# Kernel optimization log

Measured on AMD Instinct MI355X. Metric: run time of the kernel, lower is better.

## Reference

```python
import jax, jax.numpy as jnp
import numpy as np

B, T, H = 16, 2048, 1024

def setup_inputs() -> dict:
    key = jax.random.key(0)
    k1, k2, k3, k4 = jax.random.split(key, 4)
    stdv = 1.0 / np.sqrt(H)
    return {
        "hidden": jax.random.normal(k1, (B, H), dtype=jnp.float32),
        "encoder_outputs": jax.random.normal(k2, (B, T, 2 * H), dtype=jnp.float32),
        "W": jax.random.normal(k3, (H, 3 * H), dtype=jnp.float32) * stdv,  # nn.Linear(3H, H) weight
        "b": jnp.zeros((H,), dtype=jnp.float32),
        "v": jax.random.normal(k4, (H,), dtype=jnp.float32) * stdv,
    }

def reference(hidden, encoder_outputs, W, b, v):
    # hidden: (B,H); encoder_outputs: (B,T,2H)
    Bsz, Tlen, _ = encoder_outputs.shape
    Hrep = jnp.broadcast_to(hidden[:, None, :], (Bsz, Tlen, hidden.shape[-1]))  # (B,T,H)
    cat = jnp.concatenate([Hrep, encoder_outputs], axis=2)                      # (B,T,3H)
    energy = jnp.tanh(jnp.einsum('btk,hk->bth', cat, W) + b)                    # (B,T,H)
    scores = jnp.einsum('bth,h->bt', energy, v)[:, None, :]                     # (B,1,T), == bmm(v, energy^T)
    return jax.nn.softmax(scores, axis=2)
```

## Files before the change

kernel.cpp:

```cpp
#include <hip/hip_runtime.h>
#include <cstdint>

#define B_SZ 16
#define T_SZ 2048
#define H_SZ 1024
#define K_SZ 2048
#define M_SZ (B_SZ * T_SZ)

#define BM 128
#define BN 128
#define BK 64
#define LDK 72
#define KTILES (K_SZ / BK)

typedef _Float16 half8_t __attribute__((ext_vector_type(8)));
typedef float float4_t __attribute__((ext_vector_type(4)));

__device__ __forceinline__ void glds16(const _Float16* g, _Float16* l) {
    __builtin_amdgcn_global_load_lds(
        (const __attribute__((address_space(1))) void*)g,
        (__attribute__((address_space(3))) void*)l, 16, 0, 0);
}

__global__ __launch_bounds__(256) void cvt_enc_kernel(
    const float* __restrict__ src, _Float16* __restrict__ dst) {
    size_t i = ((size_t)blockIdx.x * 256 + threadIdx.x) * 8;
    float4_t a = *(const float4_t*)(src + i);
    float4_t b = *(const float4_t*)(src + i + 4);
    half8_t h;
    h[0] = (_Float16)a[0]; h[1] = (_Float16)a[1];
    h[2] = (_Float16)a[2]; h[3] = (_Float16)a[3];
    h[4] = (_Float16)b[0]; h[5] = (_Float16)b[1];
    h[6] = (_Float16)b[2]; h[7] = (_Float16)b[3];
    *(half8_t*)(dst + i) = h;
}

__global__ __launch_bounds__(256) void cvt_w2_kernel(
    const float* __restrict__ W, _Float16* __restrict__ dst) {
    int idx8 = blockIdx.x * 256 + threadIdx.x;
    int n = idx8 >> 8, k = (idx8 & 255) * 8;
    const float* src = W + (size_t)n * 3072 + H_SZ + k;
    float4_t a = *(const float4_t*)(src);
    float4_t b = *(const float4_t*)(src + 4);
    half8_t h;
    h[0] = (_Float16)a[0]; h[1] = (_Float16)a[1];
    h[2] = (_Float16)a[2]; h[3] = (_Float16)a[3];
    h[4] = (_Float16)b[0]; h[5] = (_Float16)b[1];
    h[6] = (_Float16)b[2]; h[7] = (_Float16)b[3];
    int nblk = n >> 4, m16 = n & 15;
    int kblk = k >> 5, quad = (k >> 3) & 3;
    size_t di = (((size_t)nblk * 64 + kblk) * 64 + quad * 16 + m16) * 8;
    *(half8_t*)(dst + di) = h;
}

__global__ __launch_bounds__(256) void hpart_kernel(
    const float* __restrict__ hidden, const float* __restrict__ W,
    const float* __restrict__ bias, float* __restrict__ hpart) {
    int wave = (blockIdx.x * 256 + threadIdx.x) >> 6;
    int lane = threadIdx.x & 63;
    int b = wave >> 10;
    int h = wave & 1023;
    const float* wrow = W + (size_t)h * 3072;
    const float* hrow = hidden + b * H_SZ;
    int k0 = lane * 16;
    float acc = 0.f;
#pragma unroll
    for (int j = 0; j < 4; ++j) {
        float4_t wv = *(const float4_t*)(wrow + k0 + j * 4);
        float4_t hv = *(const float4_t*)(hrow + k0 + j * 4);
        acc += wv[0] * hv[0] + wv[1] * hv[1] + wv[2] * hv[2] + wv[3] * hv[3];
    }
#pragma unroll
    for (int off = 32; off >= 1; off >>= 1) acc += __shfl_xor(acc, off, 64);
    if (lane == 0) hpart[b * H_SZ + h] = acc + bias[h];
}

__global__ __launch_bounds__(256, 4) void attn_gemm16_kernel(
    const _Float16* __restrict__ A, const _Float16* __restrict__ Bp,
    const float* __restrict__ hpart, const float* __restrict__ v,
    float* __restrict__ partial) {
    __shared__ _Float16 Af[BM * BK];
    __shared__ float hp_s[BN];
    __shared__ float v_s[BN];

    const int bidx = blockIdx.x;
    const int blockN = bidx & 7;
    const int blockM = bidx >> 3;
    const int tid = threadIdx.x;
    const int lane = tid & 63;
    const int w = tid >> 6;
    const int wm = w & 1, wn = w >> 1;
    const int m16 = lane & 15, quad = lane >> 4;
    const int sw = m16 & 7;

    const int n0 = blockN * BN;
    const int batch = blockM >> 4;

    if (tid < BN) {
        hp_s[tid] = hpart[batch * H_SZ + n0 + tid];
        v_s[tid] = v[n0 + tid];
    }

    float4_t acc[4][4];
#pragma unroll
    for (int i = 0; i < 4; ++i)
#pragma unroll
        for (int j = 0; j < 4; ++j) acc[i][j] = (float4_t){0.f, 0.f, 0.f, 0.f};

    const _Float16* Abase = A + (size_t)(blockM * BM) * K_SZ;
    const _Float16* Bfr = Bp + (((size_t)(blockN * 8 + wn * 4) * 64) * 64 + lane) * 8;

    const int r_s = tid >> 3;
    const int jcol = (((tid & 7) ^ ((tid >> 3) & 7))) * 8;

    for (int kt = 0; kt < KTILES; ++kt) {
        __syncthreads();
        const _Float16* As = Abase + kt * BK + jcol;
#pragma unroll
        for (int i = 0; i < 4; ++i) {
            int slot = i * 256 + tid;
            glds16(As + (size_t)(r_s + i * 32) * K_SZ, &Af[slot * 8]);
        }
        half8_t bfrag[2][4];
#pragma unroll
        for (int ks = 0; ks < 2; ++ks)
#pragma unroll
            for (int tn = 0; tn < 4; ++tn)
                bfrag[ks][tn] = *(const half8_t*)(
                    Bfr + (size_t)tn * (64 * 64 * 8) + (size_t)(kt * 2 + ks) * (64 * 8));
        __syncthreads();
#pragma unroll
        for (int ks = 0; ks < 2; ++ks) {
            half8_t afrag[4];
#pragma unroll
            for (int tm = 0; tm < 4; ++tm) {
                int r = wm * 64 + tm * 16 + m16;
                int p = ((ks * 4 + quad) ^ sw) * 8;
                afrag[tm] = *(const half8_t*)&Af[r * BK + p];
            }
#pragma unroll
            for (int tm = 0; tm < 4; ++tm)
#pragma unroll
                for (int tn = 0; tn < 4; ++tn)
                    acc[tm][tn] = __builtin_amdgcn_mfma_f32_16x16x32_f16(
                        afrag[tm], bfrag[ks][tn], acc[tm][tn], 0, 0, 0);
        }
    }

    const int slice = blockN * 2 + wn;
#pragma unroll
    for (int tm = 0; tm < 4; ++tm) {
        float s0 = 0.f, s1 = 0.f, s2 = 0.f, s3 = 0.f;
#pragma unroll
        for (int tn = 0; tn < 4; ++tn) {
            int nl = wn * 64 + tn * 16 + m16;
            float hpv = hp_s[nl];
            float vv = v_s[nl];
            s0 += tanhf(acc[tm][tn][0] + hpv) * vv;
            s1 += tanhf(acc[tm][tn][1] + hpv) * vv;
            s2 += tanhf(acc[tm][tn][2] + hpv) * vv;
            s3 += tanhf(acc[tm][tn][3] + hpv) * vv;
        }
#pragma unroll
        for (int off = 1; off < 16; off <<= 1) {
            s0 += __shfl_xor(s0, off, 64);
            s1 += __shfl_xor(s1, off, 64);
            s2 += __shfl_xor(s2, off, 64);
            s3 += __shfl_xor(s3, off, 64);
        }
        if (m16 == 0) {
            int gm = blockM * BM + wm * 64 + tm * 16 + quad * 4;
            float* dst = partial + (size_t)slice * M_SZ + gm;
            dst[0] = s0; dst[1] = s1; dst[2] = s2; dst[3] = s3;
        }
    }
}

__global__ __launch_bounds__(256, 2) void attn_gemm_kernel(
    const float* __restrict__ enc, const float* __restrict__ W,
    const float* __restrict__ hpart, const float* __restrict__ v,
    float* __restrict__ partial) {
    __shared__ _Float16 Af[BM * LDK];
    __shared__ _Float16 Bf[BN * LDK];
    __shared__ float hp_s[BN];
    __shared__ float v_s[BN];

    const int bidx = blockIdx.x;
    const int blockN = bidx & 7;
    const int blockM = bidx >> 3;
    const int tid = threadIdx.x;
    const int lane = tid & 63;
    const int w = tid >> 6;
    const int wm = w & 1, wn = w >> 1;
    const int m16 = lane & 15, quad = lane >> 4;

    const int n0 = blockN * BN;
    const int batch = blockM >> 4;

    if (tid < BN) {
        hp_s[tid] = hpart[batch * H_SZ + n0 + tid];
        v_s[tid] = v[n0 + tid];
    }

    float4_t acc[4][4];
#pragma unroll
    for (int i = 0; i < 4; ++i)
#pragma unroll
        for (int j = 0; j < 4; ++j) acc[i][j] = (float4_t){0.f, 0.f, 0.f, 0.f};

    const float* Abase = enc + (size_t)(blockM * BM) * K_SZ;
    const float* Bbase = W + (size_t)n0 * 3072 + H_SZ;

    for (int kt = 0; kt < KTILES; ++kt) {
        __syncthreads();
        const float* Asrc0 = Abase + kt * BK;
#pragma unroll
        for (int i = 0; i < 4; ++i) {
            int f8 = i * 256 + tid;
            int r = f8 >> 3, c8 = f8 & 7;
            const float* src = Asrc0 + (size_t)r * K_SZ + c8 * 8;
            float4_t lo = *(const float4_t*)(src);
            float4_t hi = *(const float4_t*)(src + 4);
            half8_t hv;
            hv[0] = (_Float16)lo[0]; hv[1] = (_Float16)lo[1];
            hv[2] = (_Float16)lo[2]; hv[3] = (_Float16)lo[3];
            hv[4] = (_Float16)hi[0]; hv[5] = (_Float16)hi[1];
            hv[6] = (_Float16)hi[2]; hv[7] = (_Float16)hi[3];
            *(half8_t*)&Af[r * LDK + c8 * 8] = hv;
        }
        const float* Bsrc0 = Bbase + kt * BK;
#pragma unroll
        for (int i = 0; i < 4; ++i) {
            int f8 = i * 256 + tid;
            int r = f8 >> 3, c8 = f8 & 7;
            const float* src = Bsrc0 + (size_t)r * 3072 + c8 * 8;
            float4_t lo = *(const float4_t*)(src);
            float4_t hi = *(const float4_t*)(src + 4);
            half8_t hv;
            hv[0] = (_Float16)lo[0]; hv[1] = (_Float16)lo[1];
            hv[2] = (_Float16)lo[2]; hv[3] = (_Float16)lo[3];
            hv[4] = (_Float16)hi[0]; hv[5] = (_Float16)hi[1];
            hv[6] = (_Float16)hi[2]; hv[7] = (_Float16)hi[3];
            *(half8_t*)&Bf[r * LDK + c8 * 8] = hv;
        }
        __syncthreads();
#pragma unroll
        for (int ks = 0; ks < 2; ++ks) {
            half8_t afrag[4], bfrag[4];
#pragma unroll
            for (int tm = 0; tm < 4; ++tm)
                afrag[tm] = *(const half8_t*)&Af[(wm * 64 + tm * 16 + m16) * LDK + ks * 32 + quad * 8];
#pragma unroll
            for (int tn = 0; tn < 4; ++tn)
                bfrag[tn] = *(const half8_t*)&Bf[(wn * 64 + tn * 16 + m16) * LDK + ks * 32 + quad * 8];
#pragma unroll
            for (int tm = 0; tm < 4; ++tm)
#pragma unroll
                for (int tn = 0; tn < 4; ++tn)
                    acc[tm][tn] = __builtin_amdgcn_mfma_f32_16x16x32_f16(
                        afrag[tm], bfrag[tn], acc[tm][tn], 0, 0, 0);
        }
    }

    const int slice = blockN * 2 + wn;
#pragma unroll
    for (int tm = 0; tm < 4; ++tm) {
        float s0 = 0.f, s1 = 0.f, s2 = 0.f, s3 = 0.f;
#pragma unroll
        for (int tn = 0; tn < 4; ++tn) {
            int nl = wn * 64 + tn * 16 + m16;
            float hpv = hp_s[nl];
            float vv = v_s[nl];
            s0 += tanhf(acc[tm][tn][0] + hpv) * vv;
            s1 += tanhf(acc[tm][tn][1] + hpv) * vv;
            s2 += tanhf(acc[tm][tn][2] + hpv) * vv;
            s3 += tanhf(acc[tm][tn][3] + hpv) * vv;
        }
#pragma unroll
        for (int off = 1; off < 16; off <<= 1) {
            s0 += __shfl_xor(s0, off, 64);
            s1 += __shfl_xor(s1, off, 64);
            s2 += __shfl_xor(s2, off, 64);
            s3 += __shfl_xor(s3, off, 64);
        }
        if (m16 == 0) {
            int gm = blockM * BM + wm * 64 + tm * 16 + quad * 4;
            float* dst = partial + (size_t)slice * M_SZ + gm;
            dst[0] = s0; dst[1] = s1; dst[2] = s2; dst[3] = s3;
        }
    }
}

__global__ __launch_bounds__(256) void softmax_kernel(
    const float* __restrict__ partial, float* __restrict__ out) {
    __shared__ float red[256];
    const int b = blockIdx.x;
    const int tid = threadIdx.x;
    float sc[8];
    float mymax = -1e30f;
#pragma unroll
    for (int i = 0; i < 8; ++i) {
        int t = i * 256 + tid;
        float s = 0.f;
#pragma unroll
        for (int sl = 0; sl < 16; ++sl) s += partial[(size_t)sl * M_SZ + b * T_SZ + t];
        sc[i] = s;
        mymax = fmaxf(mymax, s);
    }
    red[tid] = mymax;
    __syncthreads();
    for (int off = 128; off >= 1; off >>= 1) {
        if (tid < off) red[tid] = fmaxf(red[tid], red[tid + off]);
        __syncthreads();
    }
    float mx = red[0];
    __syncthreads();
    float mysum = 0.f;
#pragma unroll
    for (int i = 0; i < 8; ++i) {
        sc[i] = expf(sc[i] - mx);
        mysum += sc[i];
    }
    red[tid] = mysum;
    __syncthreads();
    for (int off = 128; off >= 1; off >>= 1) {
        if (tid < off) red[tid] += red[tid + off];
        __syncthreads();
    }
    float inv = 1.0f / red[0];
#pragma unroll
    for (int i = 0; i < 8; ++i) out[b * T_SZ + i * 256 + tid] = sc[i] * inv;
}

extern "C" void kernel_launch(void* const* d_in, const int* in_sizes, int n_in,
                              void* d_out, int out_size, void* d_ws, size_t ws_size,
                              hipStream_t stream) {
    const float* hidden = (const float*)d_in[0];
    const float* enc    = (const float*)d_in[1];
    const float* W      = (const float*)d_in[2];
    const float* bias   = (const float*)d_in[3];
    const float* v      = (const float*)d_in[4];
    float* out = (float*)d_out;

    float* hpart   = (float*)d_ws;
    float* partial = hpart + B_SZ * H_SZ;
    _Float16* w2h  = (_Float16*)(partial + 16 * M_SZ);
    _Float16* e16  = w2h + (size_t)H_SZ * K_SZ;
    const size_t need = (size_t)((char*)(e16 + (size_t)M_SZ * K_SZ) - (char*)d_ws);

    hipLaunchKernelGGL(hpart_kernel, dim3(4096), dim3(256), 0, stream,
                       hidden, W, bias, hpart);
    if (ws_size >= need) {
        hipLaunchKernelGGL(cvt_enc_kernel, dim3(32768), dim3(256), 0, stream, enc, e16);
        hipLaunchKernelGGL(cvt_w2_kernel, dim3(1024), dim3(256), 0, stream, W, w2h);
        hipLaunchKernelGGL(attn_gemm16_kernel, dim3(2048), dim3(256), 0, stream,
                           e16, w2h, hpart, v, partial);
    } else {
        hipLaunchKernelGGL(attn_gemm_kernel, dim3(2048), dim3(256), 0, stream,
                           enc, W, hpart, v, partial);
    }
    hipLaunchKernelGGL(softmax_kernel, dim3(B_SZ), dim3(256), 0, stream,
                       partial, out);
}
```

Baseline: 565.5 us.

## Fuse fp32-to-fp16 encoder conversion into a full-N GEMM block with in-block score reduction

Drops the separate pass that converted the encoder outputs to fp16. The new kernel loads the fp32 encoder tile, converts it in registers and writes it to a double-buffered, swizzled LDS tile. Each 1024-thread block now covers all 1024 output columns for 64 rows, so the tanh·v scores are reduced inside the block and a single score vector is written instead of 16 partial slices. This removes a 256MB fp32 read plus 128MB fp16 write-and-reread round trip and the partial-slice traffic. In exchange, occupancy per CU is lower, every wave streams B fragments from global memory each k-step, and only 512 blocks are launched.

```diff
diff --git a/kernel.cpp b/kernel.cpp
--- a/kernel.cpp
+++ b/kernel.cpp
@@ -13,27 +13,12 @@
 #define LDK 72
 #define KTILES (K_SZ / BK)
 
+#define FBM 64
+#define FBK 64
+
 typedef _Float16 half8_t __attribute__((ext_vector_type(8)));
+typedef _Float16 half4_t __attribute__((ext_vector_type(4)));
 typedef float float4_t __attribute__((ext_vector_type(4)));
-
-__device__ __forceinline__ void glds16(const _Float16* g, _Float16* l) {
-    __builtin_amdgcn_global_load_lds(
-        (const __attribute__((address_space(1))) void*)g,
-        (__attribute__((address_space(3))) void*)l, 16, 0, 0);
-}
-
-__global__ __launch_bounds__(256) void cvt_enc_kernel(
-    const float* __restrict__ src, _Float16* __restrict__ dst) {
-    size_t i = ((size_t)blockIdx.x * 256 + threadIdx.x) * 8;
-    float4_t a = *(const float4_t*)(src + i);
-    float4_t b = *(const float4_t*)(src + i + 4);
-    half8_t h;
-    h[0] = (_Float16)a[0]; h[1] = (_Float16)a[1];
-    h[2] = (_Float16)a[2]; h[3] = (_Float16)a[3];
-    h[4] = (_Float16)b[0]; h[5] = (_Float16)b[1];
-    h[6] = (_Float16)b[2]; h[7] = (_Float16)b[3];
-    *(half8_t*)(dst + i) = h;
-}
 
 __global__ __launch_bounds__(256) void cvt_w2_kernel(
     const float* __restrict__ W, _Float16* __restrict__ dst) {
@@ -75,85 +60,103 @@
     if (lane == 0) hpart[b * H_SZ + h] = acc + bias[h];
 }
 
-__global__ __launch_bounds__(256, 4) void attn_gemm16_kernel(
-    const _Float16* __restrict__ A, const _Float16* __restrict__ Bp,
+__global__ __launch_bounds__(1024) void fused_attn_kernel(
+    const float* __restrict__ enc, const _Float16* __restrict__ Bp,
     const float* __restrict__ hpart, const float* __restrict__ v,
-    float* __restrict__ partial) {
-    __shared__ _Float16 Af[BM * BK];
-    __shared__ float hp_s[BN];
-    __shared__ float v_s[BN];
-
-    const int bidx = blockIdx.x;
-    const int blockN = bidx & 7;
-    const int blockM = bidx >> 3;
+    float* __restrict__ scores) {
+    __shared__ __align__(16) _Float16 Af[2][FBM * FBK];
+    __shared__ float hp_s[H_SZ];
+    __shared__ float v_s[H_SZ];
+    __shared__ float sred[8][FBM];
+
     const int tid = threadIdx.x;
     const int lane = tid & 63;
     const int w = tid >> 6;
-    const int wm = w & 1, wn = w >> 1;
+    const int wn = w & 7;
+    const int wmg = w >> 3;
     const int m16 = lane & 15, quad = lane >> 4;
-    const int sw = m16 & 7;
-
-    const int n0 = blockN * BN;
-    const int batch = blockM >> 4;
-
-    if (tid < BN) {
-        hp_s[tid] = hpart[batch * H_SZ + n0 + tid];
-        v_s[tid] = v[n0 + tid];
-    }
-
-    float4_t acc[4][4];
-#pragma unroll
-    for (int i = 0; i < 4; ++i)
-#pragma unroll
-        for (int j = 0; j < 4; ++j) acc[i][j] = (float4_t){0.f, 0.f, 0.f, 0.f};
-
-    const _Float16* Abase = A + (size_t)(blockM * BM) * K_SZ;
-    const _Float16* Bfr = Bp + (((size_t)(blockN * 8 + wn * 4) * 64) * 64 + lane) * 8;
-
-    const int r_s = tid >> 3;
-    const int jcol = (((tid & 7) ^ ((tid >> 3) & 7))) * 8;
-
-    for (int kt = 0; kt < KTILES; ++kt) {
-        __syncthreads();
-        const _Float16* As = Abase + kt * BK + jcol;
-#pragma unroll
-        for (int i = 0; i < 4; ++i) {
-            int slot = i * 256 + tid;
-            glds16(As + (size_t)(r_s + i * 32) * K_SZ, &Af[slot * 8]);
-        }
-        half8_t bfrag[2][4];
+
+    const int blockM = blockIdx.x;
+    const int batch = blockM >> 5;
+
+    hp_s[tid] = hpart[batch * H_SZ + tid];
+    v_s[tid] = v[tid];
+
+    float4_t acc[2][8];
+#pragma unroll
+    for (int i = 0; i < 2; ++i)
+#pragma unroll
+        for (int j = 0; j < 8; ++j) acc[i][j] = (float4_t){0.f, 0.f, 0.f, 0.f};
+
+    const int arow = tid >> 4;
+    const int acq = tid & 15;
+    const float* Aptr = enc + (size_t)(blockM * FBM + arow) * K_SZ + acq * 4;
+    const int wbyte = arow * 128 + ((((acq >> 1) ^ (arow & 7)) << 4) | ((acq & 1) * 8));
+    char* AfB = (char*)Af;
+
+    int fb[2][2];
+#pragma unroll
+    for (int tm = 0; tm < 2; ++tm) {
+        int r = wmg * 32 + tm * 16 + m16;
 #pragma unroll
         for (int ks = 0; ks < 2; ++ks)
-#pragma unroll
-            for (int tn = 0; tn < 4; ++tn)
-                bfrag[ks][tn] = *(const half8_t*)(
-                    Bfr + (size_t)tn * (64 * 64 * 8) + (size_t)(kt * 2 + ks) * (64 * 8));
-        __syncthreads();
+            fb[tm][ks] = r * 128 + (((ks * 4 + quad) ^ (r & 7)) << 4);
+    }
+
+    const _Float16* Bfr = Bp + ((size_t)(wn * 8) * 64 * 64 + lane) * 8;
+
+    {
+        float4_t av = *(const float4_t*)(Aptr);
+        half4_t h;
+        h[0] = (_Float16)av[0]; h[1] = (_Float16)av[1];
+        h[2] = (_Float16)av[2]; h[3] = (_Float16)av[3];
+        *(half4_t*)(AfB + wbyte) = h;
+    }
+    __syncthreads();
+
+    int cur = 0;
+    for (int kt = 0; kt < K_SZ / FBK; ++kt) {
+        float4_t av;
+        if (kt < K_SZ / FBK - 1) av = *(const float4_t*)(Aptr + (kt + 1) * FBK);
 #pragma unroll
         for (int ks = 0; ks < 2; ++ks) {
-            half8_t afrag[4];
-#pragma unroll
-            for (int tm = 0; tm < 4; ++tm) {
-                int r = wm * 64 + tm * 16 + m16;
-                int p = ((ks * 4 + quad) ^ sw) * 8;
-                afrag[tm] = *(const half8_t*)&Af[r * BK + p];
+            half8_t af0 = *(const half8_t*)(AfB + cur * 8192 + fb[0][ks]);
+            half8_t af1 = *(const half8_t*)(AfB + cur * 8192 + fb[1][ks]);
+            const _Float16* bk = Bfr + (size_t)(kt * 2 + ks) * 512;
+#pragma unroll
+            for (int g = 0; g < 2; ++g) {
+                half8_t bf0 = *(const half8_t*)(bk + (size_t)(g * 4 + 0) * 32768);
+                half8_t bf1 = *(const half8_t*)(bk + (size_t)(g * 4 + 1) * 32768);
+                half8_t bf2 = *(const half8_t*)(bk + (size_t)(g * 4 + 2) * 32768);
+                half8_t bf3 = *(const half8_t*)(bk + (size_t)(g * 4 + 3) * 32768);
+                __builtin_amdgcn_s_setprio(1);
+                acc[0][g * 4 + 0] = __builtin_amdgcn_mfma_f32_16x16x32_f16(af0, bf0, acc[0][g * 4 + 0], 0, 0, 0);
+                acc[1][g * 4 + 0] = __builtin_amdgcn_mfma_f32_16x16x32_f16(af1, bf0, acc[1][g * 4 + 0], 0, 0, 0);
+                acc[0][g * 4 + 1] = __builtin_amdgcn_mfma_f32_16x16x32_f16(af0, bf1, acc[0][g * 4 + 1], 0, 0, 0);
+                acc[1][g * 4 + 1] = __builtin_amdgcn_mfma_f32_16x16x32_f16(af1, bf1, acc[1][g * 4 + 1], 0, 0, 0);
+                acc[0][g * 4 + 2] = __builtin_amdgcn_mfma_f32_16x16x32_f16(af0, bf2, acc[0][g * 4 + 2], 0, 0, 0);
+                acc[1][g * 4 + 2] = __builtin_amdgcn_mfma_f32_16x16x32_f16(af1, bf2, acc[1][g * 4 + 2], 0, 0, 0);
+                acc[0][g * 4 + 3] = __builtin_amdgcn_mfma_f32_16x16x32_f16(af0, bf3, acc[0][g * 4 + 3], 0, 0, 0);
+                acc[1][g * 4 + 3] = __builtin_amdgcn_mfma_f32_16x16x32_f16(af1, bf3, acc[1][g * 4 + 3], 0, 0, 0);
+                __builtin_amdgcn_s_setprio(0);
             }
-#pragma unroll
-            for (int tm = 0; tm < 4; ++tm)
-#pragma unroll
-                for (int tn = 0; tn < 4; ++tn)
-                    acc[tm][tn] = __builtin_amdgcn_mfma_f32_16x16x32_f16(
-                        afrag[tm], bfrag[ks][tn], acc[tm][tn], 0, 0, 0);
-        }
-    }
-
-    const int slice = blockN * 2 + wn;
-#pragma unroll
-    for (int tm = 0; tm < 4; ++tm) {
+        }
+        if (kt < K_SZ / FBK - 1) {
+            half4_t h;
+            h[0] = (_Float16)av[0]; h[1] = (_Float16)av[1];
+            h[2] = (_Float16)av[2]; h[3] = (_Float16)av[3];
+            *(half4_t*)(AfB + (cur ^ 1) * 8192 + wbyte) = h;
+        }
+        __syncthreads();
+        cur ^= 1;
+    }
+
+#pragma unroll
+    for (int tm = 0; tm < 2; ++tm) {
         float s0 = 0.f, s1 = 0.f, s2 = 0.f, s3 = 0.f;
 #pragma unroll
-        for (int tn = 0; tn < 4; ++tn) {
-            int nl = wn * 64 + tn * 16 + m16;
+        for (int tn = 0; tn < 8; ++tn) {
+            int nl = wn * 128 + tn * 16 + m16;
             float hpv = hp_s[nl];
             float vv = v_s[nl];
             s0 += tanhf(acc[tm][tn][0] + hpv) * vv;
@@ -169,19 +172,66 @@
             s3 += __shfl_xor(s3, off, 64);
         }
         if (m16 == 0) {
-            int gm = blockM * BM + wm * 64 + tm * 16 + quad * 4;
-            float* dst = partial + (size_t)slice * M_SZ + gm;
-            dst[0] = s0; dst[1] = s1; dst[2] = s2; dst[3] = s3;
-        }
-    }
+            int rl = wmg * 32 + tm * 16 + quad * 4;
+            sred[wn][rl + 0] = s0;
+            sred[wn][rl + 1] = s1;
+            sred[wn][rl + 2] = s2;
+            sred[wn][rl + 3] = s3;
+        }
+    }
+    __syncthreads();
+    if (tid < FBM) {
+        float t = 0.f;
+#pragma unroll
+        for (int i = 0; i < 8; ++i) t += sred[i][tid];
+        scores[(size_t)blockM * FBM + tid] = t;
+    }
+}
+
+__global__ __launch_bounds__(256) void softmax1_kernel(
+    const float* __restrict__ scores, float* __restrict__ out) {
+    __shared__ float red[256];
+    const int b = blockIdx.x;
+    const int tid = threadIdx.x;
+    float sc[8];
+    float mymax = -1e30f;
+#pragma unroll
+    for (int i = 0; i < 8; ++i) {
+        float s = scores[b * T_SZ + i * 256 + tid];
+        sc[i] = s;
+        mymax = fmaxf(mymax, s);
+    }
+    red[tid] = mymax;
+    __syncthreads();
+    for (int off = 128; off >= 1; off >>= 1) {
+        if (tid < off) red[tid] = fmaxf(red[tid], red[tid + off]);
+        __syncthreads();
+    }
+    float mx = red[0];
+    __syncthreads();
+    float mysum = 0.f;
+#pragma unroll
+    for (int i = 0; i < 8; ++i) {
+        sc[i] = expf(sc[i] - mx);
+        mysum += sc[i];
+    }
+    red[tid] = mysum;
+    __syncthreads();
+    for (int off = 128; off >= 1; off >>= 1) {
+        if (tid < off) red[tid] += red[tid + off];
+        __syncthreads();
+    }
+    float inv = 1.0f / red[0];
+#pragma unroll
+    for (int i = 0; i < 8; ++i) out[b * T_SZ + i * 256 + tid] = sc[i] * inv;
 }
 
 __global__ __launch_bounds__(256, 2) void attn_gemm_kernel(
     const float* __restrict__ enc, const float* __restrict__ W,
     const float* __restrict__ hpart, const float* __restrict__ v,
     float* __restrict__ partial) {
-    __shared__ _Float16 Af[BM * LDK];
-    __shared__ _Float16 Bf[BN * LDK];
+    __shared__ _Float16 Afs[BM * LDK];
+    __shared__ _Float16 Bfs[BN * LDK];
     __shared__ float hp_s[BN];
     __shared__ float v_s[BN];
 
@@ -226,7 +276,7 @@
             hv[2] = (_Float16)lo[2]; hv[3] = (_Float16)lo[3];
             hv[4] = (_Float16)hi[0]; hv[5] = (_Float16)hi[1];
             hv[6] = (_Float16)hi[2]; hv[7] = (_Float16)hi[3];
-            *(half8_t*)&Af[r * LDK + c8 * 8] = hv;
+            *(half8_t*)&Afs[r * LDK + c8 * 8] = hv;
         }
         const float* Bsrc0 = Bbase + kt * BK;
 #pragma unroll
@@ -241,7 +291,7 @@
             hv[2] = (_Float16)lo[2]; hv[3] = (_Float16)lo[3];
             hv[4] = (_Float16)hi[0]; hv[5] = (_Float16)hi[1];
             hv[6] = (_Float16)hi[2]; hv[7] = (_Float16)hi[3];
-            *(half8_t*)&Bf[r * LDK + c8 * 8] = hv;
+            *(half8_t*)&Bfs[r * LDK + c8 * 8] = hv;
         }
         __syncthreads();
 #pragma unroll
@@ -249,10 +299,10 @@
             half8_t afrag[4], bfrag[4];
 #pragma unroll
             for (int tm = 0; tm < 4; ++tm)
-                afrag[tm] = *(const half8_t*)&Af[(wm * 64 + tm * 16 + m16) * LDK + ks * 32 + quad * 8];
+                afrag[tm] = *(const half8_t*)&Afs[(wm * 64 + tm * 16 + m16) * LDK + ks * 32 + quad * 8];
 #pragma unroll
             for (int tn = 0; tn < 4; ++tn)
-                bfrag[tn] = *(const half8_t*)&Bf[(wn * 64 + tn * 16 + m16) * LDK + ks * 32 + quad * 8];
+                bfrag[tn] = *(const half8_t*)&Bfs[(wn * 64 + tn * 16 + m16) * LDK + ks * 32 + quad * 8];
 #pragma unroll
             for (int tm = 0; tm < 4; ++tm)
 #pragma unroll
@@ -342,23 +392,24 @@
     const float* v      = (const float*)d_in[4];
     float* out = (float*)d_out;
 
-    float* hpart   = (float*)d_ws;
-    float* partial = hpart + B_SZ * H_SZ;
-    _Float16* w2h  = (_Float16*)(partial + 16 * M_SZ);
-    _Float16* e16  = w2h + (size_t)H_SZ * K_SZ;
-    const size_t need = (size_t)((char*)(e16 + (size_t)M_SZ * K_SZ) - (char*)d_ws);
+    float* hpart  = (float*)d_ws;
+    float* scores = hpart + B_SZ * H_SZ;
+    _Float16* w2h = (_Float16*)(scores + M_SZ);
+    const size_t need = (size_t)((char*)(w2h + (size_t)H_SZ * K_SZ) - (char*)d_ws);
 
     hipLaunchKernelGGL(hpart_kernel, dim3(4096), dim3(256), 0, stream,
                        hidden, W, bias, hpart);
     if (ws_size >= need) {
-        hipLaunchKernelGGL(cvt_enc_kernel, dim3(32768), dim3(256), 0, stream, enc, e16);
         hipLaunchKernelGGL(cvt_w2_kernel, dim3(1024), dim3(256), 0, stream, W, w2h);
-        hipLaunchKernelGGL(attn_gemm16_kernel, dim3(2048), dim3(256), 0, stream,
-                           e16, w2h, hpart, v, partial);
+        hipLaunchKernelGGL(fused_attn_kernel, dim3(M_SZ / FBM), dim3(1024), 0, stream,
+                           enc, w2h, hpart, v, scores);
+        hipLaunchKernelGGL(softmax1_kernel, dim3(B_SZ), dim3(256), 0, stream,
+                           scores, out);
     } else {
+        float* partial = scores;
         hipLaunchKernelGGL(attn_gemm_kernel, dim3(2048), dim3(256), 0, stream,
                            enc, W, hpart, v, partial);
-    }
-    hipLaunchKernelGGL(softmax_kernel, dim3(B_SZ), dim3(256), 0, stream,
-                       partial, out);
-}
+        hipLaunchKernelGGL(softmax_kernel, dim3(B_SZ), dim3(256), 0, stream,
+                           partial, out);
+    }
+}
```

After: 556.4 us. No clear change (-1.6%).
